# Performance work log

Measured on AMD Instinct MI355X. Metric: run time of the kernel, lower is better.

Reference implementation:

```python
import jax, jax.numpy as jnp
import numpy as np

N_NODES = 40000
N_EDGES = 640000
IN_DIM = 128
EDGE_DIM = 64
HID = 128


def setup_inputs() -> dict:
    key = jax.random.key(0)
    ks = jax.random.split(key, 12)
    s = 0.05  # small param scale keeps exp(attention) well-behaved
    return {
        "node_features": jax.random.normal(ks[0], (N_NODES, IN_DIM), jnp.float32),
        "edge_index": jax.random.randint(ks[1], (2, N_EDGES), 0, N_NODES, jnp.int32),
        "edge_features": jax.random.normal(ks[2], (N_EDGES, EDGE_DIM), jnp.float32),
        "W_node": jax.random.normal(ks[3], (IN_DIM, HID), jnp.float32) * s,
        "b_node": jnp.zeros((HID,), jnp.float32),
        "W_edge": jax.random.normal(ks[4], (EDGE_DIM, HID), jnp.float32) * s,
        "b_edge": jnp.zeros((HID,), jnp.float32),
        "W_att1": jax.random.normal(ks[5], (3 * HID, HID), jnp.float32) * s,
        "b_att1": jnp.zeros((HID,), jnp.float32),
        "W_att2": jax.random.normal(ks[6], (HID, 1), jnp.float32) * s,
        "b_att2": jnp.zeros((1,), jnp.float32),
        "W_out": jax.random.normal(ks[7], (HID, HID), jnp.float32) * s,
        "b_out": jnp.zeros((HID,), jnp.float32),
        "ln_gamma": jnp.ones((HID,), jnp.float32),
        "ln_beta": jnp.zeros((HID,), jnp.float32),
    }


def reference(node_features, edge_index, edge_features, W_node, b_node,
              W_edge, b_edge, W_att1, b_att1, W_att2, b_att2,
              W_out, b_out, ln_gamma, ln_beta):
    N = node_features.shape[0]
    src, dst = edge_index[0], edge_index[1]
    # per-edge-type node/edge transforms
    h = node_features @ W_node + b_node          # [N, H]
    he = edge_features @ W_edge + b_edge          # [E, H]
    h_src = h[src]                                # [E, H]
    h_dst = h[dst]                                # [E, H]
    cat = jnp.concatenate([h_src, h_dst, he], axis=1)  # [E, 3H]
    att = jnp.tanh(cat @ W_att1 + b_att1) @ W_att2 + b_att2  # [E, 1]
    # softmax over edges grouped by src (unstabilized exp, matching source)
    att_exp = jnp.exp(att)
    denom = jax.ops.segment_sum(att_exp, src, num_segments=N)  # [N, 1]
    coeff = att_exp / denom[src]                  # [E, 1]
    # weighted scatter-aggregate onto src nodes
    agg = jax.ops.segment_sum(h_dst * coeff, src, num_segments=N)  # [N, H]
    # output transform: Linear -> LayerNorm -> ReLU
    o = agg @ W_out + b_out
    mu = jnp.mean(o, axis=-1, keepdims=True)
    var = jnp.mean(jnp.square(o - mu), axis=-1, keepdims=True)
    o = (o - mu) * jax.lax.rsqrt(var + 1e-5) * ln_gamma + ln_beta
    return jax.nn.relu(o)
```

## Files before the change

### kernel.cpp

```cpp
#include <hip/hip_runtime.h>
#include <math.h>

#define N_NODES 40000
#define N_EDGES 640000
#define IN_DIM 128
#define EDGE_DIM 64
#define HID 128

typedef __attribute__((ext_vector_type(8))) short bf16x8;
typedef __attribute__((ext_vector_type(4))) float f32x4;

__device__ __forceinline__ ushort f2bf(float f) {
    unsigned int x = __float_as_uint(f);
    x += 0x7fffu + ((x >> 16) & 1u);
    return (ushort)(x >> 16);
}
__device__ __forceinline__ float bf2f(ushort u) {
    return __uint_as_float(((unsigned int)u) << 16);
}
__device__ __forceinline__ float tanh_fast(float x) {
    return 1.f - __fdividef(2.f, __expf(2.f * x) + 1.f);
}

__global__ __launch_bounds__(256) void k_A(
    const float* __restrict__ W_edge, const float* __restrict__ W1,
    const float* __restrict__ b_att1, const float* __restrict__ b_edge,
    float* __restrict__ Wc, float* __restrict__ b_eff,
    const int* __restrict__ srcI, int* __restrict__ cnt)
{
    const int bid = blockIdx.x;
    if (bid < 33) {
        const float* W1he = W1 + 256 * 128;
        if (bid == 32) {
            const int n = threadIdx.x;
            if (n < 128) {
                float s = b_att1[n];
                for (int k = 0; k < 128; ++k) s = fmaf(b_edge[k], W1he[k * 128 + n], s);
                b_eff[n] = s;
            }
            return;
        }
        const int idx = bid * 256 + threadIdx.x;
        const int row = idx >> 7, n = idx & 127;
        float s = 0.f;
        for (int k = 0; k < 128; ++k) s = fmaf(W_edge[row * 128 + k], W1he[k * 128 + n], s);
        Wc[idx] = s;
    } else {
        const int e = (bid - 33) * 256 + threadIdx.x;
        atomicAdd(&cnt[srcI[e]], 1);
    }
}

__global__ __launch_bounds__(1024) void k_B(
    const float* __restrict__ W1, const float* __restrict__ Wc,
    const float* __restrict__ Wn, const float* __restrict__ Wo,
    ushort* __restrict__ packB, ushort* __restrict__ packA,
    ushort* __restrict__ packN, ushort* __restrict__ packO,
    const int* __restrict__ cnt, int* __restrict__ rowptr)
{
    const int bid = blockIdx.x;
    if (bid < 72) {
        const int idx = bid * 1024 + threadIdx.x;
        if (idx < 32768) {
            const int j = idx & 7, lane = (idx >> 3) & 63, nt = (idx >> 9) & 7, k0 = idx >> 12;
            const int k = k0 * 32 + (lane >> 4) * 8 + j;
            const int n = nt * 16 + (lane & 15);
            packB[idx] = f2bf(W1[k * 128 + n]);
        } else if (idx < 40960) {
            const int i2 = idx - 32768;
            const int j = i2 & 7, lane = (i2 >> 3) & 63, mt = (i2 >> 9) & 7, k0 = i2 >> 12;
            const int k = k0 * 32 + (lane >> 4) * 8 + j;
            const int row = mt * 16 + (lane & 15);
            packA[i2] = f2bf(Wc[k * 128 + row]);
        } else if (idx < 57344) {
            const int i3 = idx - 40960;
            const int j = i3 & 7, lane = (i3 >> 3) & 63, nt = (i3 >> 9) & 7, k0 = i3 >> 12;
            const int k = k0 * 32 + (lane >> 4) * 8 + j;
            const int n = nt * 16 + (lane & 15);
            packN[i3] = f2bf(Wn[k * 128 + n]);
        } else {
            const int i4 = idx - 57344;
            const int j = i4 & 7, lane = (i4 >> 3) & 63, nt = (i4 >> 9) & 7, k0 = i4 >> 12;
            const int k = k0 * 32 + (lane >> 4) * 8 + j;
            const int n = nt * 16 + (lane & 15);
            packO[i4] = f2bf(Wo[k * 128 + n]);
        }
        return;
    }
    __shared__ int wsum[16];
    __shared__ int carry;
    const int tid = threadIdx.x, lane = tid & 63, wid = tid >> 6;
    if (tid == 0) { carry = 0; rowptr[0] = 0; }
    __syncthreads();
    for (int base = 0; base < N_NODES; base += 4096) {
        const int i = base + tid * 4;
        int4 c = {0, 0, 0, 0};
        if (i < N_NODES) c = *reinterpret_cast<const int4*>(cnt + i);
        const int tsum = c.x + c.y + c.z + c.w;
        int v = tsum;
#pragma unroll
        for (int d = 1; d < 64; d <<= 1) {
            const int t = __shfl_up(v, d, 64);
            if (lane >= d) v += t;
        }
        if (lane == 63) wsum[wid] = v;
        __syncthreads();
        if (wid == 0 && lane < 16) {
            int w = wsum[lane];
#pragma unroll
            for (int d = 1; d < 16; d <<= 1) {
                const int t = __shfl_up(w, d, 16);
                if ((lane & 15) >= d) w += t;
            }
            wsum[lane] = w;
        }
        __syncthreads();
        const int off = (wid == 0) ? 0 : wsum[wid - 1];
        const int excl = carry + off + v - tsum;
        if (i < N_NODES) {
            rowptr[i + 1] = excl + c.x;
            rowptr[i + 2] = excl + c.x + c.y;
            rowptr[i + 3] = excl + c.x + c.y + c.z;
            rowptr[i + 4] = excl + tsum;
        }
        const int total = wsum[15];
        __syncthreads();
        if (tid == 0) carry += total;
        __syncthreads();
    }
}

__global__ __launch_bounds__(256) void k_C(
    const float* __restrict__ X, const ushort* __restrict__ packN,
    const ushort* __restrict__ packB, const float* __restrict__ b,
    const float* __restrict__ b_eff, ushort* __restrict__ Hb,
    ushort* __restrict__ G1, ushort* __restrict__ G2,
    const int* __restrict__ srcI, const int* __restrict__ dstI,
    const int* __restrict__ rowptr, int* __restrict__ cursor,
    int2* __restrict__ edrec)
{
    const int bid = blockIdx.x;
    if (bid >= 625) {
        const int e = (bid - 625) * 256 + threadIdx.x;
        const int s = srcI[e];
        const int pos = rowptr[s] + atomicAdd(&cursor[s], 1);
        int2 rec;
        rec.x = e;
        rec.y = (s << 16) | dstI[e];
        edrec[pos] = rec;
        return;
    }
    __shared__ ushort hs[4][16][144];
    const int tid = threadIdx.x;
    const int wave = tid >> 6, lane = tid & 63;
    const int r = lane & 15, g = lane >> 4;
    const int nbase = bid * 64 + wave * 16;
    const float* rowX = X + (size_t)(nbase + r) * 128 + g * 8;
    const bf16x8* BpN = reinterpret_cast<const bf16x8*>(packN);
    const bf16x8* BpB = reinterpret_cast<const bf16x8*>(packB);

    f32x4 acc[8];
#pragma unroll
    for (int nt = 0; nt < 8; ++nt) {
        const float bv = b[nt * 16 + r];
        acc[nt] = (f32x4){bv, bv, bv, bv};
    }
#pragma unroll
    for (int k0 = 0; k0 < 4; ++k0) {
        const float4 u0 = *reinterpret_cast<const float4*>(rowX + k0 * 32);
        const float4 u1 = *reinterpret_cast<const float4*>(rowX + k0 * 32 + 4);
        bf16x8 a;
        a[0] = (short)f2bf(u0.x); a[1] = (short)f2bf(u0.y);
        a[2] = (short)f2bf(u0.z); a[3] = (short)f2bf(u0.w);
        a[4] = (short)f2bf(u1.x); a[5] = (short)f2bf(u1.y);
        a[6] = (short)f2bf(u1.z); a[7] = (short)f2bf(u1.w);
#pragma unroll
        for (int nt = 0; nt < 8; ++nt)
            acc[nt] = __builtin_amdgcn_mfma_f32_16x16x32_bf16(
                a, BpN[(k0 * 8 + nt) * 64 + lane], acc[nt], 0, 0, 0);
    }
#pragma unroll
    for (int nt = 0; nt < 8; ++nt) {
#pragma unroll
        for (int q = 0; q < 4; ++q) {
            const ushort bv = f2bf(acc[nt][q]);
            Hb[(size_t)(nbase + g * 4 + q) * 128 + nt * 16 + r] = bv;
            hs[wave][g * 4 + q][nt * 16 + r] = bv;
        }
    }

    bf16x8 afr[4];
#pragma unroll
    for (int k0 = 0; k0 < 4; ++k0)
        afr[k0] = *reinterpret_cast<const bf16x8*>(&hs[wave][r][k0 * 32 + g * 8]);

    const int coff = (r >> 2) * 32 + (r & 3);

#pragma unroll
    for (int nt = 0; nt < 8; ++nt) acc[nt] = (f32x4){0.f, 0.f, 0.f, 0.f};
#pragma unroll
    for (int k0 = 0; k0 < 4; ++k0) {
#pragma unroll
        for (int nt = 0; nt < 8; ++nt)
            acc[nt] = __builtin_amdgcn_mfma_f32_16x16x32_bf16(
                afr[k0], BpB[(k0 * 8 + nt) * 64 + lane], acc[nt], 0, 0, 0);
    }
#pragma unroll
    for (int nt = 0; nt < 8; ++nt) {
        const float bv = b_eff[nt * 16 + r];
#pragma unroll
        for (int q = 0; q < 4; ++q)
            G1[(size_t)(nbase + g * 4 + q) * 128 + coff + nt * 4] = f2bf(acc[nt][q] + bv);
    }

#pragma unroll
    for (int nt = 0; nt < 8; ++nt) acc[nt] = (f32x4){0.f, 0.f, 0.f, 0.f};
#pragma unroll
    for (int k0 = 0; k0 < 4; ++k0) {
#pragma unroll
        for (int nt = 0; nt < 8; ++nt)
            acc[nt] = __builtin_amdgcn_mfma_f32_16x16x32_bf16(
                afr[k0], BpB[((k0 + 4) * 8 + nt) * 64 + lane], acc[nt], 0, 0, 0);
    }
#pragma unroll
    for (int nt = 0; nt < 8; ++nt) {
#pragma unroll
        for (int q = 0; q < 4; ++q)
            G2[(size_t)(nbase + g * 4 + q) * 128 + coff + nt * 4] = f2bf(acc[nt][q]);
    }
}

__global__ __launch_bounds__(256) void k_edge_att_v10(
    const int2* __restrict__ edrec, const float* __restrict__ EF,
    const ushort* __restrict__ G1, const ushort* __restrict__ G2,
    const ushort* __restrict__ packA,
    const float* __restrict__ W2, const float* __restrict__ b2,
    float* __restrict__ csr_p)
{
    const int tid = threadIdx.x;
    const int wave = tid >> 6, lane = tid & 63;
    const int r = lane & 15, g = lane >> 4;
    const int pbase = blockIdx.x * 64 + wave * 16;
    const int pos = pbase + r;
    const int2 rec = edrec[pos];
    const int e = rec.x;
    const int di = rec.y & 0xffff;
    const int si = ((unsigned)rec.y) >> 16;

    const ushort* g2base = G2 + (size_t)di * 128 + g * 32;
    bf16x8 g2r[4];
#pragma unroll
    for (int m2 = 0; m2 < 4; ++m2)
        g2r[m2] = *reinterpret_cast<const bf16x8*>(g2base + m2 * 8);

    const ushort* g1base = G1 + (size_t)si * 128 + g * 32;
    f32x4 acc[8];
#pragma unroll
    for (int m2 = 0; m2 < 4; ++m2) {
        const bf16x8 a = *reinterpret_cast<const bf16x8*>(g1base + m2 * 8);
#pragma unroll
        for (int q = 0; q < 4; ++q) {
            acc[2 * m2][q]     = bf2f((ushort)a[q]);
            acc[2 * m2 + 1][q] = bf2f((ushort)a[4 + q]);
        }
    }

    const float* rowE = EF + (size_t)e * 64 + g * 8;
    bf16x8 b0, b1;
    {
        const float4 u0 = *reinterpret_cast<const float4*>(rowE);
        const float4 u1 = *reinterpret_cast<const float4*>(rowE + 4);
        b0[0] = (short)f2bf(u0.x); b0[1] = (short)f2bf(u0.y);
        b0[2] = (short)f2bf(u0.z); b0[3] = (short)f2bf(u0.w);
        b0[4] = (short)f2bf(u1.x); b0[5] = (short)f2bf(u1.y);
        b0[6] = (short)f2bf(u1.z); b0[7] = (short)f2bf(u1.w);
        const float4 v0 = *reinterpret_cast<const float4*>(rowE + 32);
        const float4 v1 = *reinterpret_cast<const float4*>(rowE + 36);
        b1[0] = (short)f2bf(v0.x); b1[1] = (short)f2bf(v0.y);
        b1[2] = (short)f2bf(v0.z); b1[3] = (short)f2bf(v0.w);
        b1[4] = (short)f2bf(v1.x); b1[5] = (short)f2bf(v1.y);
        b1[6] = (short)f2bf(v1.z); b1[7] = (short)f2bf(v1.w);
    }

    const bf16x8* Ap = reinterpret_cast<const bf16x8*>(packA);
#pragma unroll
    for (int mt = 0; mt < 8; ++mt)
        acc[mt] = __builtin_amdgcn_mfma_f32_16x16x32_bf16(
            Ap[(0 * 8 + mt) * 64 + lane], b0, acc[mt], 0, 0, 0);
#pragma unroll
    for (int mt = 0; mt < 8; ++mt)
        acc[mt] = __builtin_amdgcn_mfma_f32_16x16x32_bf16(
            Ap[(1 * 8 + mt) * 64 + lane], b1, acc[mt], 0, 0, 0);

    float part = 0.f;
#pragma unroll
    for (int mt = 0; mt < 8; ++mt) {
        const bf16x8 gr = g2r[mt >> 1];
        const int h4 = (mt & 1) * 4;
        const float4 w2v = *reinterpret_cast<const float4*>(W2 + mt * 16 + g * 4);
        const float z0 = acc[mt][0] + bf2f((ushort)gr[h4 + 0]);
        const float z1 = acc[mt][1] + bf2f((ushort)gr[h4 + 1]);
        const float z2 = acc[mt][2] + bf2f((ushort)gr[h4 + 2]);
        const float z3 = acc[mt][3] + bf2f((ushort)gr[h4 + 3]);
        part = fmaf(tanh_fast(z0), w2v.x, part);
        part = fmaf(tanh_fast(z1), w2v.y, part);
        part = fmaf(tanh_fast(z2), w2v.z, part);
        part = fmaf(tanh_fast(z3), w2v.w, part);
    }
    part += __shfl_xor(part, 16, 64);
    part += __shfl_xor(part, 32, 64);
    if (lane < 16) csr_p[pos] = __expf(part + b2[0]);
}

__global__ __launch_bounds__(256) void k_agg(
    const int* __restrict__ rowptr, const float* __restrict__ csr_p,
    const int2* __restrict__ edrec, const ushort* __restrict__ Hb,
    ushort* __restrict__ AGGb)
{
    const int tid = threadIdx.x;
    const int wave = tid >> 6, lane = tid & 63;
    const int slot = lane >> 4, tc = lane & 15;
    const int n = blockIdx.x * 4 + wave;
    const int beg = rowptr[n], end = rowptr[n + 1];

    float v[8];
#pragma unroll
    for (int i = 0; i < 8; ++i) v[i] = 0.f;
    float sp = 0.f;

    int j = beg + slot;
    for (; j + 4 < end; j += 8) {
        const float p0 = csr_p[j];
        const int d0 = edrec[j].y & 0xffff;
        const float p1 = csr_p[j + 4];
        const int d1 = edrec[j + 4].y & 0xffff;
        const bf16x8 h0 = *reinterpret_cast<const bf16x8*>(Hb + (size_t)d0 * 128 + tc * 8);
        const bf16x8 h1 = *reinterpret_cast<const bf16x8*>(Hb + (size_t)d1 * 128 + tc * 8);
#pragma unroll
        for (int i = 0; i < 8; ++i) {
            v[i] = fmaf(p0, bf2f((ushort)h0[i]), v[i]);
            v[i] = fmaf(p1, bf2f((ushort)h1[i]), v[i]);
        }
        sp += p0 + p1;
    }
    for (; j < end; j += 4) {
        const float p = csr_p[j];
        const int d = edrec[j].y & 0xffff;
        const bf16x8 hv = *reinterpret_cast<const bf16x8*>(Hb + (size_t)d * 128 + tc * 8);
#pragma unroll
        for (int i = 0; i < 8; ++i) v[i] = fmaf(p, bf2f((ushort)hv[i]), v[i]);
        sp += p;
    }
#pragma unroll
    for (int m = 16; m <= 32; m <<= 1) {
#pragma unroll
        for (int i = 0; i < 8; ++i) v[i] += __shfl_xor(v[i], m, 64);
        sp += __shfl_xor(sp, m, 64);
    }
    if (lane < 16) {
        const float inv = (end > beg) ? 1.f / sp : 0.f;
        bf16x8 o;
#pragma unroll
        for (int i = 0; i < 8; ++i) o[i] = (short)f2bf(v[i] * inv);
        *reinterpret_cast<bf16x8*>(AGGb + (size_t)n * 128 + tc * 8) = o;
    }
}

__global__ __launch_bounds__(256) void k_out_ln(
    const ushort* __restrict__ AGGb, const ushort* __restrict__ packO,
    const float* __restrict__ b, const float* __restrict__ gamma,
    const float* __restrict__ beta, float* __restrict__ OUT)
{
    const int tid = threadIdx.x;
    const int wave = tid >> 6, lane = tid & 63;
    const int r = lane & 15, g = lane >> 4;
    const int nbase = blockIdx.x * 64 + wave * 16;
    const ushort* rowA = AGGb + (size_t)(nbase + r) * 128 + g * 8;
    const bf16x8* Bp = reinterpret_cast<const bf16x8*>(packO);

    f32x4 acc[8];
#pragma unroll
    for (int nt = 0; nt < 8; ++nt) {
        const float bv = b[nt * 16 + r];
        acc[nt] = (f32x4){bv, bv, bv, bv};
    }
#pragma unroll
    for (int k0 = 0; k0 < 4; ++k0) {
        const bf16x8 a = *reinterpret_cast<const bf16x8*>(rowA + k0 * 32);
#pragma unroll
        for (int nt = 0; nt < 8; ++nt)
            acc[nt] = __builtin_amdgcn_mfma_f32_16x16x32_bf16(
                a, Bp[(k0 * 8 + nt) * 64 + lane], acc[nt], 0, 0, 0);
    }

    float s1[4] = {0.f, 0.f, 0.f, 0.f};
    float s2[4] = {0.f, 0.f, 0.f, 0.f};
#pragma unroll
    for (int nt = 0; nt < 8; ++nt) {
#pragma unroll
        for (int q = 0; q < 4; ++q) {
            const float z = acc[nt][q];
            s1[q] += z;
            s2[q] = fmaf(z, z, s2[q]);
        }
    }
#pragma unroll
    for (int m = 1; m <= 8; m <<= 1) {
#pragma unroll
        for (int q = 0; q < 4; ++q) {
            s1[q] += __shfl_xor(s1[q], m, 64);
            s2[q] += __shfl_xor(s2[q], m, 64);
        }
    }
    float mu[4], rr[4];
#pragma unroll
    for (int q = 0; q < 4; ++q) {
        mu[q] = s1[q] * (1.f / 128.f);
        const float var = s2[q] * (1.f / 128.f) - mu[q] * mu[q];
        rr[q] = rsqrtf(var + 1e-5f);
    }
#pragma unroll
    for (int nt = 0; nt < 8; ++nt) {
        const int col = nt * 16 + r;
        const float ga = gamma[col], be = beta[col];
#pragma unroll
        for (int q = 0; q < 4; ++q) {
            const float o = (acc[nt][q] - mu[q]) * rr[q] * ga + be;
            OUT[(size_t)(nbase + g * 4 + q) * 128 + col] = o > 0.f ? o : 0.f;
        }
    }
}

extern "C" void kernel_launch(void* const* d_in, const int* in_sizes, int n_in,
                              void* d_out, int out_size, void* d_ws, size_t ws_size,
                              hipStream_t stream)
{
    const float* node_features = (const float*)d_in[0];
    const int*   edge_index    = (const int*)d_in[1];
    const float* edge_features = (const float*)d_in[2];
    const float* W_node  = (const float*)d_in[3];
    const float* b_node  = (const float*)d_in[4];
    const float* W_edge  = (const float*)d_in[5];
    const float* b_edge  = (const float*)d_in[6];
    const float* W_att1  = (const float*)d_in[7];
    const float* b_att1  = (const float*)d_in[8];
    const float* W_att2  = (const float*)d_in[9];
    const float* b_att2  = (const float*)d_in[10];
    const float* W_out   = (const float*)d_in[11];
    const float* b_out   = (const float*)d_in[12];
    const float* ln_gamma = (const float*)d_in[13];
    const float* ln_beta  = (const float*)d_in[14];
    float* out = (float*)d_out;

    char* ws = (char*)d_ws;
    ushort* hb      = (ushort*)(ws);
    ushort* G1      = (ushort*)(ws + 10240000);
    ushort* G2      = (ushort*)(ws + 20480000);
    ushort* aggb    = (ushort*)(ws + 30720000);
    float*  csr_p   = (float*)(ws + 40960000);
    int2*   edrec   = (int2*)(ws + 43520000);
    int*    rowptr  = (int*)(ws + 48640000);
    int*    cnt     = (int*)(ws + 48800016);
    int*    cursor  = (int*)(ws + 48960016);
    float*  Wc      = (float*)(ws + 49120016);
    float*  b_eff   = (float*)(ws + 49152784);
    ushort* packB   = (ushort*)(ws + 49153296);
    ushort* packA   = (ushort*)(ws + 49218832);
    ushort* packN   = (ushort*)(ws + 49235216);
    ushort* packO   = (ushort*)(ws + 49267984);

    const int* srcI = edge_index;
    const int* dstI = edge_index + N_EDGES;

    hipMemsetAsync(cnt, 0, 320000, stream);

    k_A<<<2533, 256, 0, stream>>>(W_edge, W_att1, b_att1, b_edge, Wc, b_eff,
                                  srcI, cnt);
    k_B<<<73, 1024, 0, stream>>>(W_att1, Wc, W_node, W_out,
                                 packB, packA, packN, packO, cnt, rowptr);
    k_C<<<3125, 256, 0, stream>>>(node_features, packN, packB, b_node, b_eff,
                                  hb, G1, G2, srcI, dstI, rowptr, cursor, edrec);
    k_edge_att_v10<<<N_EDGES / 64, 256, 0, stream>>>(edrec, edge_features,
                                                     G1, G2, packA, W_att2, b_att2,
                                                     csr_p);
    k_agg<<<N_NODES / 4, 256, 0, stream>>>(rowptr, csr_p, edrec, hb, aggb);
    k_out_ln<<<N_NODES / 64, 256, 0, stream>>>(aggb, packO, b_out, ln_gamma, ln_beta, out);
}
```

Measured before the change: 207.6 us.

## Precompute h@W_out per node and fuse output LayerNorm into aggregation

Because the softmax coefficients sum to one per node, agg@W_out equals the weighted sum of (h@W_out) rows. The node-transform kernel now computes G3 = h@W_out with an extra MFMA pass, and the aggregation kernel gathers G3 rows, normalises them, adds the bias and applies LayerNorm and ReLU directly. This removes the separate output GEMM kernel and the bf16 AGG round trip through memory. The Hb buffer is no longer written. Nodes with no outgoing edges still get b_out since inv is zero. Rounding changes because h@W_out is computed from bf16 h and stored in bf16 before aggregation.

```diff
diff --git a/kernel.cpp b/kernel.cpp
--- a/kernel.cpp
+++ b/kernel.cpp
@@ -132,9 +132,9 @@
 
 __global__ __launch_bounds__(256) void k_C(
     const float* __restrict__ X, const ushort* __restrict__ packN,
-    const ushort* __restrict__ packB, const float* __restrict__ b,
-    const float* __restrict__ b_eff, ushort* __restrict__ Hb,
-    ushort* __restrict__ G1, ushort* __restrict__ G2,
+    const ushort* __restrict__ packB, const ushort* __restrict__ packO,
+    const float* __restrict__ b, const float* __restrict__ b_eff,
+    ushort* __restrict__ G1, ushort* __restrict__ G2, ushort* __restrict__ G3,
     const int* __restrict__ srcI, const int* __restrict__ dstI,
     const int* __restrict__ rowptr, int* __restrict__ cursor,
     int2* __restrict__ edrec)
@@ -158,6 +158,7 @@
     const float* rowX = X + (size_t)(nbase + r) * 128 + g * 8;
     const bf16x8* BpN = reinterpret_cast<const bf16x8*>(packN);
     const bf16x8* BpB = reinterpret_cast<const bf16x8*>(packB);
+    const bf16x8* BpO = reinterpret_cast<const bf16x8*>(packO);
 
     f32x4 acc[8];
 #pragma unroll
@@ -182,11 +183,8 @@
 #pragma unroll
     for (int nt = 0; nt < 8; ++nt) {
 #pragma unroll
-        for (int q = 0; q < 4; ++q) {
-            const ushort bv = f2bf(acc[nt][q]);
-            Hb[(size_t)(nbase + g * 4 + q) * 128 + nt * 16 + r] = bv;
-            hs[wave][g * 4 + q][nt * 16 + r] = bv;
-        }
+        for (int q = 0; q < 4; ++q)
+            hs[wave][g * 4 + q][nt * 16 + r] = f2bf(acc[nt][q]);
     }
 
     bf16x8 afr[4];
@@ -227,6 +225,22 @@
 #pragma unroll
         for (int q = 0; q < 4; ++q)
             G2[(size_t)(nbase + g * 4 + q) * 128 + coff + nt * 4] = f2bf(acc[nt][q]);
+    }
+
+#pragma unroll
+    for (int nt = 0; nt < 8; ++nt) acc[nt] = (f32x4){0.f, 0.f, 0.f, 0.f};
+#pragma unroll
+    for (int k0 = 0; k0 < 4; ++k0) {
+#pragma unroll
+        for (int nt = 0; nt < 8; ++nt)
+            acc[nt] = __builtin_amdgcn_mfma_f32_16x16x32_bf16(
+                afr[k0], BpO[(k0 * 8 + nt) * 64 + lane], acc[nt], 0, 0, 0);
+    }
+#pragma unroll
+    for (int nt = 0; nt < 8; ++nt) {
+#pragma unroll
+        for (int q = 0; q < 4; ++q)
+            G3[(size_t)(nbase + g * 4 + q) * 128 + nt * 16 + r] = f2bf(acc[nt][q]);
     }
 }
 
@@ -314,8 +328,9 @@
 
 __global__ __launch_bounds__(256) void k_agg(
     const int* __restrict__ rowptr, const float* __restrict__ csr_p,
-    const int2* __restrict__ edrec, const ushort* __restrict__ Hb,
-    ushort* __restrict__ AGGb)
+    const int2* __restrict__ edrec, const ushort* __restrict__ G3,
+    const float* __restrict__ b_out, const float* __restrict__ gamma,
+    const float* __restrict__ beta, float* __restrict__ OUT)
 {
     const int tid = threadIdx.x;
     const int wave = tid >> 6, lane = tid & 63;
@@ -334,8 +349,8 @@
         const int d0 = edrec[j].y & 0xffff;
         const float p1 = csr_p[j + 4];
         const int d1 = edrec[j + 4].y & 0xffff;
-        const bf16x8 h0 = *reinterpret_cast<const bf16x8*>(Hb + (size_t)d0 * 128 + tc * 8);
-        const bf16x8 h1 = *reinterpret_cast<const bf16x8*>(Hb + (size_t)d1 * 128 + tc * 8);
+        const bf16x8 h0 = *reinterpret_cast<const bf16x8*>(G3 + (size_t)d0 * 128 + tc * 8);
+        const bf16x8 h1 = *reinterpret_cast<const bf16x8*>(G3 + (size_t)d1 * 128 + tc * 8);
 #pragma unroll
         for (int i = 0; i < 8; ++i) {
             v[i] = fmaf(p0, bf2f((ushort)h0[i]), v[i]);
@@ -346,7 +361,7 @@
     for (; j < end; j += 4) {
         const float p = csr_p[j];
         const int d = edrec[j].y & 0xffff;
-        const bf16x8 hv = *reinterpret_cast<const bf16x8*>(Hb + (size_t)d * 128 + tc * 8);
+        const bf16x8 hv = *reinterpret_cast<const bf16x8*>(G3 + (size_t)d * 128 + tc * 8);
 #pragma unroll
         for (int i = 0; i < 8; ++i) v[i] = fmaf(p, bf2f((ushort)hv[i]), v[i]);
         sp += p;
@@ -357,77 +372,49 @@
         for (int i = 0; i < 8; ++i) v[i] += __shfl_xor(v[i], m, 64);
         sp += __shfl_xor(sp, m, 64);
     }
+
+    const float inv = (end > beg) ? 1.f / sp : 0.f;
+    const float4 bo0 = *reinterpret_cast<const float4*>(b_out + tc * 8);
+    const float4 bo1 = *reinterpret_cast<const float4*>(b_out + tc * 8 + 4);
+    float x[8];
+    x[0] = fmaf(v[0], inv, bo0.x); x[1] = fmaf(v[1], inv, bo0.y);
+    x[2] = fmaf(v[2], inv, bo0.z); x[3] = fmaf(v[3], inv, bo0.w);
+    x[4] = fmaf(v[4], inv, bo1.x); x[5] = fmaf(v[5], inv, bo1.y);
+    x[6] = fmaf(v[6], inv, bo1.z); x[7] = fmaf(v[7], inv, bo1.w);
+
+    float s1 = 0.f, s2 = 0.f;
+#pragma unroll
+    for (int i = 0; i < 8; ++i) { s1 += x[i]; s2 = fmaf(x[i], x[i], s2); }
+#pragma unroll
+    for (int m = 1; m <= 8; m <<= 1) {
+        s1 += __shfl_xor(s1, m, 64);
+        s2 += __shfl_xor(s2, m, 64);
+    }
+    const float mu = s1 * (1.f / 128.f);
+    const float var = s2 * (1.f / 128.f) - mu * mu;
+    const float rr = rsqrtf(var + 1e-5f);
+
     if (lane < 16) {
-        const float inv = (end > beg) ? 1.f / sp : 0.f;
-        bf16x8 o;
-#pragma unroll
-        for (int i = 0; i < 8; ++i) o[i] = (short)f2bf(v[i] * inv);
-        *reinterpret_cast<bf16x8*>(AGGb + (size_t)n * 128 + tc * 8) = o;
-    }
-}
-
-__global__ __launch_bounds__(256) void k_out_ln(
-    const ushort* __restrict__ AGGb, const ushort* __restrict__ packO,
-    const float* __restrict__ b, const float* __restrict__ gamma,
-    const float* __restrict__ beta, float* __restrict__ OUT)
-{
-    const int tid = threadIdx.x;
-    const int wave = tid >> 6, lane = tid & 63;
-    const int r = lane & 15, g = lane >> 4;
-    const int nbase = blockIdx.x * 64 + wave * 16;
-    const ushort* rowA = AGGb + (size_t)(nbase + r) * 128 + g * 8;
-    const bf16x8* Bp = reinterpret_cast<const bf16x8*>(packO);
-
-    f32x4 acc[8];
-#pragma unroll
-    for (int nt = 0; nt < 8; ++nt) {
-        const float bv = b[nt * 16 + r];
-        acc[nt] = (f32x4){bv, bv, bv, bv};
-    }
-#pragma unroll
-    for (int k0 = 0; k0 < 4; ++k0) {
-        const bf16x8 a = *reinterpret_cast<const bf16x8*>(rowA + k0 * 32);
-#pragma unroll
-        for (int nt = 0; nt < 8; ++nt)
-            acc[nt] = __builtin_amdgcn_mfma_f32_16x16x32_bf16(
-                a, Bp[(k0 * 8 + nt) * 64 + lane], acc[nt], 0, 0, 0);
-    }
-
-    float s1[4] = {0.f, 0.f, 0.f, 0.f};
-    float s2[4] = {0.f, 0.f, 0.f, 0.f};
-#pragma unroll
-    for (int nt = 0; nt < 8; ++nt) {
-#pragma unroll
-        for (int q = 0; q < 4; ++q) {
-            const float z = acc[nt][q];
-            s1[q] += z;
-            s2[q] = fmaf(z, z, s2[q]);
-        }
-    }
-#pragma unroll
-    for (int m = 1; m <= 8; m <<= 1) {
-#pragma unroll
-        for (int q = 0; q < 4; ++q) {
-            s1[q] += __shfl_xor(s1[q], m, 64);
-            s2[q] += __shfl_xor(s2[q], m, 64);
-        }
-    }
-    float mu[4], rr[4];
-#pragma unroll
-    for (int q = 0; q < 4; ++q) {
-        mu[q] = s1[q] * (1.f / 128.f);
-        const float var = s2[q] * (1.f / 128.f) - mu[q] * mu[q];
-        rr[q] = rsqrtf(var + 1e-5f);
-    }
-#pragma unroll
-    for (int nt = 0; nt < 8; ++nt) {
-        const int col = nt * 16 + r;
-        const float ga = gamma[col], be = beta[col];
-#pragma unroll
-        for (int q = 0; q < 4; ++q) {
-            const float o = (acc[nt][q] - mu[q]) * rr[q] * ga + be;
-            OUT[(size_t)(nbase + g * 4 + q) * 128 + col] = o > 0.f ? o : 0.f;
-        }
+        const float4 ga0 = *reinterpret_cast<const float4*>(gamma + tc * 8);
+        const float4 ga1 = *reinterpret_cast<const float4*>(gamma + tc * 8 + 4);
+        const float4 be0 = *reinterpret_cast<const float4*>(beta + tc * 8);
+        const float4 be1 = *reinterpret_cast<const float4*>(beta + tc * 8 + 4);
+        float4 o0, o1;
+        o0.x = (x[0] - mu) * rr * ga0.x + be0.x;
+        o0.y = (x[1] - mu) * rr * ga0.y + be0.y;
+        o0.z = (x[2] - mu) * rr * ga0.z + be0.z;
+        o0.w = (x[3] - mu) * rr * ga0.w + be0.w;
+        o1.x = (x[4] - mu) * rr * ga1.x + be1.x;
+        o1.y = (x[5] - mu) * rr * ga1.y + be1.y;
+        o1.z = (x[6] - mu) * rr * ga1.z + be1.z;
+        o1.w = (x[7] - mu) * rr * ga1.w + be1.w;
+        o0.x = o0.x > 0.f ? o0.x : 0.f; o0.y = o0.y > 0.f ? o0.y : 0.f;
+        o0.z = o0.z > 0.f ? o0.z : 0.f; o0.w = o0.w > 0.f ? o0.w : 0.f;
+        o1.x = o1.x > 0.f ? o1.x : 0.f; o1.y = o1.y > 0.f ? o1.y : 0.f;
+        o1.z = o1.z > 0.f ? o1.z : 0.f; o1.w = o1.w > 0.f ? o1.w : 0.f;
+        float* orow = OUT + (size_t)n * 128 + tc * 8;
+        *reinterpret_cast<float4*>(orow) = o0;
+        *reinterpret_cast<float4*>(orow + 4) = o1;
     }
 }
 
@@ -453,10 +440,9 @@
     float* out = (float*)d_out;
 
     char* ws = (char*)d_ws;
-    ushort* hb      = (ushort*)(ws);
+    ushort* G3      = (ushort*)(ws);
     ushort* G1      = (ushort*)(ws + 10240000);
     ushort* G2      = (ushort*)(ws + 20480000);
-    ushort* aggb    = (ushort*)(ws + 30720000);
     float*  csr_p   = (float*)(ws + 40960000);
     int2*   edrec   = (int2*)(ws + 43520000);
     int*    rowptr  = (int*)(ws + 48640000);
@@ -478,11 +464,12 @@
                                   srcI, cnt);
     k_B<<<73, 1024, 0, stream>>>(W_att1, Wc, W_node, W_out,
                                  packB, packA, packN, packO, cnt, rowptr);
-    k_C<<<3125, 256, 0, stream>>>(node_features, packN, packB, b_node, b_eff,
-                                  hb, G1, G2, srcI, dstI, rowptr, cursor, edrec);
+    k_C<<<3125, 256, 0, stream>>>(node_features, packN, packB, packO,
+                                  b_node, b_eff, G1, G2, G3,
+                                  srcI, dstI, rowptr, cursor, edrec);
     k_edge_att_v10<<<N_EDGES / 64, 256, 0, stream>>>(edrec, edge_features,
                                                      G1, G2, packA, W_att2, b_att2,
                                                      csr_p);
-    k_agg<<<N_NODES / 4, 256, 0, stream>>>(rowptr, csr_p, edrec, hb, aggb);
-    k_out_ln<<<N_NODES / 64, 256, 0, stream>>>(aggb, packO, b_out, ln_gamma, ln_beta, out);
-}
+    k_agg<<<N_NODES / 4, 256, 0, stream>>>(rowptr, csr_p, edrec, G3,
+                                           b_out, ln_gamma, ln_beta, out);
+}
```

New measurement: 212.6 us (median of 2 runs). +2.4%, slower.
